# Optimization experiments

Hardware: AMD Instinct MI355X
Metric: run time of the kernel (lower is better)

## Reference

```python
import jax, jax.numpy as jnp
import numpy as np

N = 100000      # num nodes
E = 1600000     # num edges
F_IN = 128
F_OUT = 128
BN_EPS = 1e-5


def setup_inputs() -> dict:
    key = jax.random.key(0)
    ks = jax.random.split(key, 8)
    x = jax.random.normal(ks[0], (N, F_IN), dtype=jnp.float32)
    edge_index = jax.random.randint(ks[1], (2, E), 0, N, dtype=jnp.int64)
    # GIN learnable epsilon (init 0.0)
    eps = jnp.zeros((), dtype=jnp.float32)
    # MLP: Linear(F_IN->F_OUT) -> BatchNorm1d -> ReLU -> Linear(F_OUT->F_OUT)
    lim1 = 1.0 / np.sqrt(F_IN)
    W1 = jax.random.uniform(ks[2], (F_OUT, F_IN), minval=-lim1, maxval=lim1, dtype=jnp.float32)
    b1 = jax.random.uniform(ks[3], (F_OUT,), minval=-lim1, maxval=lim1, dtype=jnp.float32)
    gamma = jnp.ones((F_OUT,), dtype=jnp.float32)
    beta = jnp.zeros((F_OUT,), dtype=jnp.float32)
    lim2 = 1.0 / np.sqrt(F_OUT)
    W2 = jax.random.uniform(ks[4], (F_OUT, F_OUT), minval=-lim2, maxval=lim2, dtype=jnp.float32)
    b2 = jax.random.uniform(ks[5], (F_OUT,), minval=-lim2, maxval=lim2, dtype=jnp.float32)
    return {"x": x, "edge_index": edge_index, "eps": eps,
            "W1": W1, "b1": b1, "gamma": gamma, "beta": beta,
            "W2": W2, "b2": b2}


def reference(x, edge_index, eps, W1, b1, gamma, beta, W2, b2):
    row, col = edge_index[0], edge_index[1]
    # gather neighbor features and scatter-add into destination nodes
    agg = jax.ops.segment_sum(x[col], row, num_segments=x.shape[0])  # [N, F_IN]
    h = (1.0 + eps) * x + agg
    # Linear 1
    h = h @ W1.T + b1  # [N, F_OUT]
    # BatchNorm1d (training mode: batch stats over nodes, biased variance)
    mu = jnp.mean(h, axis=0)
    var = jnp.mean(jnp.square(h - mu), axis=0)
    h = (h - mu) * jax.lax.rsqrt(var + BN_EPS) * gamma + beta
    h = jax.nn.relu(h)
    # Linear 2
    return h @ W2.T + b2
```

## Files before the change

### kernel.cpp

```cpp
#include <hip/hip_runtime.h>


#define F 128
#define NPB 64

typedef __attribute__((ext_vector_type(8))) short short8;
typedef __attribute__((ext_vector_type(4))) float float4v;

__device__ inline float b2f(unsigned short u) {
    union { unsigned int i; float f; } v; v.i = ((unsigned int)u) << 16; return v.f;
}
__device__ inline unsigned short f2b(float f) {
    union { float f; unsigned int i; } v; v.f = f;
    unsigned int r = v.i + 0x7FFFu + ((v.i >> 16) & 1u);
    return (unsigned short)(r >> 16);
}

__global__ __launch_bounds__(256) void conv_kernel(const float* __restrict__ x,
                                                   unsigned short* __restrict__ xh, int total,
                                                   const float* __restrict__ W1,
                                                   const float* __restrict__ W2,
                                                   unsigned short* __restrict__ w1h,
                                                   unsigned short* __restrict__ w2h,
                                                   int* __restrict__ bucketCnt, int nbuk,
                                                   float* __restrict__ stats) {
    int t = blockIdx.x * 256 + threadIdx.x;
    int i = t * 8;
    if (i < total) {
        float4 v0 = *(const float4*)(x + i);
        float4 v1 = *(const float4*)(x + i + 4);
        short8 o;
        o[0] = (short)f2b(v0.x); o[1] = (short)f2b(v0.y); o[2] = (short)f2b(v0.z); o[3] = (short)f2b(v0.w);
        o[4] = (short)f2b(v1.x); o[5] = (short)f2b(v1.y); o[6] = (short)f2b(v1.z); o[7] = (short)f2b(v1.w);
        *(short8*)(xh + i) = o;
    }
    if (t < F * F) {
        w1h[t] = f2b(W1[t]);
        w2h[t] = f2b(W2[t]);
    }
    if (blockIdx.x == 0) {
        for (int k = threadIdx.x; k < nbuk; k += 256) bucketCnt[k] = 0;
    } else if (blockIdx.x == 1) {
        if (threadIdx.x < 256) stats[threadIdx.x] = 0.f;
    }
}

__global__ __launch_bounds__(256) void bucket_hist_kernel(const int* __restrict__ rows,
                                                          int* __restrict__ bucketCnt,
                                                          int E, int nbuk) {
    extern __shared__ int bh[];
    int tid = threadIdx.x;
    for (int i = tid; i < nbuk; i += 256) bh[i] = 0;
    __syncthreads();
    int stride = gridDim.x * 256;
    for (int i = blockIdx.x * 256 + tid; i < E; i += stride)
        atomicAdd(&bh[rows[i] >> 6], 1);
    __syncthreads();
    for (int b = tid; b < nbuk; b += 256) {
        int c = bh[b];
        if (c) atomicAdd(&bucketCnt[b], c);
    }
}

__global__ void scan_buckets_kernel(const int* __restrict__ bucketCnt, int* __restrict__ bOffs,
                                    int* __restrict__ gcursor, int nbuk) {
    const int SEG = 7;
    __shared__ int tmp[256];
    int t = threadIdx.x;
    int base = t * SEG;
    int v[SEG], s = 0;
#pragma unroll
    for (int j = 0; j < SEG; j++) {
        int idx = base + j;
        v[j] = (idx < nbuk) ? bucketCnt[idx] : 0;
        s += v[j];
    }
    tmp[t] = s;
    __syncthreads();
    for (int off = 1; off < 256; off <<= 1) {
        int u = (t >= off) ? tmp[t - off] : 0;
        __syncthreads();
        tmp[t] += u;
        __syncthreads();
    }
    int run = tmp[t] - s;
#pragma unroll
    for (int j = 0; j < SEG; j++) {
        int idx = base + j;
        if (idx < nbuk) { bOffs[idx] = run; gcursor[idx] = run; }
        run += v[j];
    }
    if (t == 255) bOffs[nbuk] = tmp[255];
}

__global__ __launch_bounds__(1024) void binned_scatter_kernel(const int* __restrict__ rows,
                                                              const int* __restrict__ cols,
                                                              int* __restrict__ gcursor,
                                                              int* __restrict__ recbuf,
                                                              int E, int nbuk) {
    extern __shared__ int sm[];
    int* bh = sm;
    int* gb = sm + nbuk;
    int tid = threadIdx.x;
    int chunk = (E + gridDim.x - 1) / gridDim.x;
    int e0 = blockIdx.x * chunk;
    int e1 = min(E, e0 + chunk);
    for (int i = tid; i < nbuk; i += 1024) bh[i] = 0;
    __syncthreads();
    for (int i = e0 + tid; i < e1; i += 1024)
        atomicAdd(&bh[rows[i] >> 6], 1);
    __syncthreads();
    for (int b = tid; b < nbuk; b += 1024) {
        int c = bh[b];
        gb[b] = c ? atomicAdd(&gcursor[b], c) : 0;
        bh[b] = 0;
    }
    __syncthreads();
    for (int i = e0 + tid; i < e1; i += 1024) {
        int r = rows[i], c = cols[i];
        int k = r >> 6;
        int rk = atomicAdd(&bh[k], 1);
        recbuf[gb[k] + rk] = (c << 6) | (r & 63);
    }
}

__global__ __launch_bounds__(256) void bucket_sort_kernel(const int* __restrict__ recbuf,
                                                          const int* __restrict__ bOffs,
                                                          int* __restrict__ clist,
                                                          int* __restrict__ offs,
                                                          int n, int nbuk) {
    __shared__ int hist[NPB];
    __shared__ int cur[NPB];
    int b = blockIdx.x, tid = threadIdx.x;
    int base = bOffs[b];
    int cnt = bOffs[b + 1] - base;
    if (tid < NPB) hist[tid] = 0;
    __syncthreads();
    for (int i = tid; i < cnt; i += 256) atomicAdd(&hist[recbuf[base + i] & 63], 1);
    __syncthreads();
    if (tid < 64) {
        int h = hist[tid], v = h;
#pragma unroll
        for (int off = 1; off < 64; off <<= 1) {
            int u = __shfl_up(v, off, 64);
            if (tid >= off) v += u;
        }
        cur[tid] = v - h;
        int g = b * NPB + tid;
        if (g < n) offs[g] = base + v - h;
    }
    if (b == 0 && tid == 0) offs[n] = bOffs[nbuk];
    __syncthreads();
    for (int i = tid; i < cnt; i += 256) {
        int r = recbuf[base + i];
        int p = atomicAdd(&cur[r & 63], 1);
        clist[base + p] = r >> 6;
    }
}

__global__ __launch_bounds__(256) void agg_kernel(const unsigned short* __restrict__ xh,
                                                  const int* __restrict__ offs,
                                                  const int* __restrict__ clist,
                                                  const float* __restrict__ epsPtr,
                                                  unsigned short* __restrict__ h0h,
                                                  int base_node, int n_end) {
    int wave = threadIdx.x >> 6, lane = threadIdx.x & 63;
    int node = base_node + blockIdx.x * 4 + wave;
    if (node >= n_end) return;
    int qt = lane >> 4;
    int c16 = lane & 15;
    const short8* xh8 = (const short8*)xh;
    float acc[8];
#pragma unroll
    for (int j = 0; j < 8; j++) acc[j] = 0.f;
    int s = offs[node], e = offs[node + 1];
    int i = s;
    for (; i + 16 <= e; i += 16) {
        int c[4];
#pragma unroll
        for (int u = 0; u < 4; u++) c[u] = clist[i + 4 * u + qt];
        short8 v[4];
#pragma unroll
        for (int u = 0; u < 4; u++) v[u] = xh8[(size_t)c[u] * 16 + c16];
#pragma unroll
        for (int u = 0; u < 4; u++)
#pragma unroll
            for (int j = 0; j < 8; j++) acc[j] += b2f((unsigned short)v[u][j]);
    }
    if (i < e) {
        int c[4];
#pragma unroll
        for (int u = 0; u < 4; u++) {
            int idx = i + 4 * u + qt;
            c[u] = (idx < e) ? clist[idx] : -1;
        }
        short8 v[4];
#pragma unroll
        for (int u = 0; u < 4; u++)
            v[u] = xh8[(size_t)(c[u] < 0 ? 0 : c[u]) * 16 + c16];
#pragma unroll
        for (int u = 0; u < 4; u++) {
            if (c[u] >= 0) {
#pragma unroll
                for (int j = 0; j < 8; j++) acc[j] += b2f((unsigned short)v[u][j]);
            }
        }
    }
#pragma unroll
    for (int j = 0; j < 8; j++) {
        acc[j] += __shfl_xor(acc[j], 16, 64);
        acc[j] += __shfl_xor(acc[j], 32, 64);
    }
    if (qt == 0) {
        float sc = 1.0f + epsPtr[0];
        short8 xv = xh8[(size_t)node * 16 + c16];
        short8 o;
#pragma unroll
        for (int j = 0; j < 8; j++) {
            float r = fmaf(sc, b2f((unsigned short)xv[j]), acc[j]);
            o[j] = (short)f2b(r);
        }
        ((short8*)h0h)[(size_t)node * 16 + c16] = o;
    }
}

#define WLD 136
__global__ __launch_bounds__(256, 2) void gemm1_mfma_kernel(const unsigned short* __restrict__ h0h,
                                                            const unsigned short* __restrict__ w1h,
                                                            const float* __restrict__ b1,
                                                            unsigned short* __restrict__ h1h,
                                                            float* __restrict__ partials, int n) {
    __shared__ unsigned short wl[128 * WLD];
    __shared__ float red[4 * 256];
    int tid = threadIdx.x;
    for (int i = tid; i < 128 * 16; i += 256) {
        int r = i >> 4, ch = i & 15;
        *(short8*)(wl + r * WLD + ch * 8) = *(const short8*)(w1h + r * 128 + ch * 8);
    }
    __syncthreads();

    int wv = tid >> 6, lane = tid & 63;
    int q = lane >> 4, c15 = lane & 15;
    int rowbase = blockIdx.x * 64 + wv * 16;
    int arow = rowbase + c15; if (arow >= n) arow = n - 1;
    const unsigned short* aptr = h0h + (size_t)arow * 128 + q * 8;

    float4v acc[8];
#pragma unroll
    for (int nt = 0; nt < 8; nt++) {
        float bb = b1[nt * 16 + c15];
        acc[nt] = (float4v){bb, bb, bb, bb};
    }
#pragma unroll
    for (int ks = 0; ks < 4; ks++) {
        short8 a = *(const short8*)(aptr + ks * 32);
        const unsigned short* wp = wl + q * 8 + ks * 32;
#pragma unroll
        for (int nt = 0; nt < 8; nt++) {
            short8 b = *(const short8*)(wp + (nt * 16 + c15) * WLD);
            acc[nt] = __builtin_amdgcn_mfma_f32_16x16x32_bf16(a, b, acc[nt], 0, 0, 0);
        }
    }

    float sum[8], sq[8];
#pragma unroll
    for (int nt = 0; nt < 8; nt++) {
        sum[nt] = 0.f; sq[nt] = 0.f;
#pragma unroll
        for (int r = 0; r < 4; r++) {
            int row = rowbase + q * 4 + r;
            if (row < n) {
                float v = acc[nt][r];
                h1h[(size_t)row * 128 + nt * 16 + c15] = f2b(v);
                sum[nt] += v; sq[nt] += v * v;
            }
        }
        sum[nt] += __shfl_xor(sum[nt], 16, 64);
        sum[nt] += __shfl_xor(sum[nt], 32, 64);
        sq[nt]  += __shfl_xor(sq[nt], 16, 64);
        sq[nt]  += __shfl_xor(sq[nt], 32, 64);
    }
    if (lane < 16) {
#pragma unroll
        for (int nt = 0; nt < 8; nt++) {
            red[wv * 256 + nt * 16 + c15] = sum[nt];
            red[wv * 256 + 128 + nt * 16 + c15] = sq[nt];
        }
    }
    __syncthreads();
    if (wv == 0) {
        float* pout = partials + (size_t)blockIdx.x * 256;
        for (int c = lane; c < 128; c += 64) {
            float S = red[c] + red[256 + c] + red[512 + c] + red[768 + c];
            float Q = red[128 + c] + red[384 + c] + red[640 + c] + red[896 + c];
            pout[c] = S;
            pout[128 + c] = Q;
        }
    }
}

__global__ __launch_bounds__(256) void bn_reduce_kernel(const float* __restrict__ partials,
                                                        float* __restrict__ stats, int nb) {
    int t = threadIdx.x;
    int per = (nb + gridDim.x - 1) / gridDim.x;
    int j0 = blockIdx.x * per, j1 = min(nb, j0 + per);
    float s = 0.f;
    for (int j = j0; j < j1; j++) s += partials[(size_t)j * 256 + t];
    atomicAdd(&stats[t], s);
}

__global__ __launch_bounds__(256, 2) void gemm2_mfma_kernel(const unsigned short* __restrict__ h1h,
                                                            const unsigned short* __restrict__ w2h,
                                                            const float* __restrict__ b2,
                                                            const float* __restrict__ stats,
                                                            const float* __restrict__ gamma,
                                                            const float* __restrict__ beta,
                                                            float* __restrict__ out, int n) {
    __shared__ unsigned short wl[128 * WLD];
    __shared__ float ssl[256];
    int tid = threadIdx.x;
    for (int i = tid; i < 128 * 16; i += 256) {
        int r = i >> 4, ch = i & 15;
        *(short8*)(wl + r * WLD + ch * 8) = *(const short8*)(w2h + r * 128 + ch * 8);
    }
    if (tid < 128) {
        float inv_n = 1.0f / (float)n;
        float mu = stats[tid] * inv_n;
        float var = stats[F + tid] * inv_n - mu * mu;
        var = fmaxf(var, 0.0f);
        float rs = rsqrtf(var + 1e-5f);
        float s = gamma[tid] * rs;
        ssl[tid] = s;
        ssl[F + tid] = beta[tid] - mu * s;
    }
    __syncthreads();

    int wv = tid >> 6, lane = tid & 63;
    int q = lane >> 4, c15 = lane & 15;
    int rowbase = blockIdx.x * 64 + wv * 16;
    int arow = rowbase + c15; if (arow >= n) arow = n - 1;
    const unsigned short* aptr = h1h + (size_t)arow * 128 + q * 8;

    float4v acc[8];
#pragma unroll
    for (int nt = 0; nt < 8; nt++) {
        float bb = b2[nt * 16 + c15];
        acc[nt] = (float4v){bb, bb, bb, bb};
    }
#pragma unroll
    for (int ks = 0; ks < 4; ks++) {
        short8 araw = *(const short8*)(aptr + ks * 32);
        const float* ssp = ssl + ks * 32 + q * 8;
        float4 s0 = *(const float4*)(ssp);
        float4 s1 = *(const float4*)(ssp + 4);
        float4 t0 = *(const float4*)(ssp + 128);
        float4 t1 = *(const float4*)(ssp + 132);
        short8 a;
        a[0] = (short)f2b(fmaxf(fmaf(b2f((unsigned short)araw[0]), s0.x, t0.x), 0.f));
        a[1] = (short)f2b(fmaxf(fmaf(b2f((unsigned short)araw[1]), s0.y, t0.y), 0.f));
        a[2] = (short)f2b(fmaxf(fmaf(b2f((unsigned short)araw[2]), s0.z, t0.z), 0.f));
        a[3] = (short)f2b(fmaxf(fmaf(b2f((unsigned short)araw[3]), s0.w, t0.w), 0.f));
        a[4] = (short)f2b(fmaxf(fmaf(b2f((unsigned short)araw[4]), s1.x, t1.x), 0.f));
        a[5] = (short)f2b(fmaxf(fmaf(b2f((unsigned short)araw[5]), s1.y, t1.y), 0.f));
        a[6] = (short)f2b(fmaxf(fmaf(b2f((unsigned short)araw[6]), s1.z, t1.z), 0.f));
        a[7] = (short)f2b(fmaxf(fmaf(b2f((unsigned short)araw[7]), s1.w, t1.w), 0.f));
        const unsigned short* wp = wl + q * 8 + ks * 32;
#pragma unroll
        for (int nt = 0; nt < 8; nt++) {
            short8 b = *(const short8*)(wp + (nt * 16 + c15) * WLD);
            acc[nt] = __builtin_amdgcn_mfma_f32_16x16x32_bf16(a, b, acc[nt], 0, 0, 0);
        }
    }
#pragma unroll
    for (int nt = 0; nt < 8; nt++) {
#pragma unroll
        for (int r = 0; r < 4; r++) {
            int row = rowbase + q * 4 + r;
            if (row < n)
                out[(size_t)row * 128 + nt * 16 + c15] = acc[nt][r];
        }
    }
}

extern "C" void kernel_launch(void* const* d_in, const int* in_sizes, int n_in,
                              void* d_out, int out_size, void* d_ws, size_t ws_size,
                              hipStream_t stream) {
    const float* x     = (const float*)d_in[0];
    const int*   ei    = (const int*)d_in[1];
    const float* eps   = (const float*)d_in[2];
    const float* W1    = (const float*)d_in[3];
    const float* b1    = (const float*)d_in[4];
    const float* gamma = (const float*)d_in[5];
    const float* beta  = (const float*)d_in[6];
    const float* W2    = (const float*)d_in[7];
    const float* b2    = (const float*)d_in[8];
    float* out = (float*)d_out;

    const int E = in_sizes[1] / 2;
    const int n = in_sizes[0] / F;
    const int nbuk = (n + NPB - 1) / NPB;
    const int ntiles = (n + 63) / 64;

    char* w = (char*)d_ws;
    auto alloc = [&](size_t bytes) -> void* {
        void* p = (void*)w;
        w += (bytes + 255) & ~(size_t)255;
        return p;
    };
    int*            bucketCnt = (int*)alloc((size_t)nbuk * 4);
    int*            bOffs     = (int*)alloc((size_t)(nbuk + 1) * 4);
    int*            gcursor   = (int*)alloc((size_t)nbuk * 4);
    int*            offs      = (int*)alloc((size_t)(n + 1) * 4);
    float*          stats     = (float*)alloc(256 * 4);
    float*          partials  = (float*)alloc((size_t)ntiles * 256 * 4);
    unsigned short* w1h       = (unsigned short*)alloc(F * F * 2);
    unsigned short* w2h       = (unsigned short*)alloc(F * F * 2);
    int*            recbuf    = (int*)alloc((size_t)E * 4);
    int*            clist     = (int*)alloc((size_t)E * 4);
    unsigned short* xh        = (unsigned short*)alloc((size_t)n * F * 2);
    unsigned short* h0h       = (unsigned short*)alloc((size_t)n * F * 2);
    unsigned short* h1h       = (unsigned short*)alloc((size_t)n * F * 2);

    const int* rows = ei;
    const int* cols = ei + E;

    conv_kernel<<<(n * F / 8 + 255) / 256, 256, 0, stream>>>(x, xh, n * F, W1, W2, w1h, w2h,
                                                             bucketCnt, nbuk, stats);
    bucket_hist_kernel<<<256, 256, nbuk * 4, stream>>>(rows, bucketCnt, E, nbuk);
    scan_buckets_kernel<<<1, 256, 0, stream>>>(bucketCnt, bOffs, gcursor, nbuk);
    binned_scatter_kernel<<<128, 1024, nbuk * 8, stream>>>(rows, cols, gcursor, recbuf, E, nbuk);
    bucket_sort_kernel<<<nbuk, 256, 0, stream>>>(recbuf, bOffs, clist, offs, n, nbuk);

    int nhalf = n / 2;
    agg_kernel<<<(nhalf + 3) / 4, 256, 0, stream>>>(xh, offs, clist, eps, h0h, 0, nhalf);
    agg_kernel<<<(n - nhalf + 3) / 4, 256, 0, stream>>>(xh, offs, clist, eps, h0h, nhalf, n);

    gemm1_mfma_kernel<<<ntiles, 256, 0, stream>>>(h0h, w1h, b1, h1h, partials, n);
    bn_reduce_kernel<<<16, 256, 0, stream>>>(partials, stats, ntiles);
    gemm2_mfma_kernel<<<ntiles, 256, 0, stream>>>(h1h, w2h, b2, stats, gamma, beta, out, n);
}
```

Measured before the change: 294.6 us.

## Replace two-level bucket sort CSR build with direct global-atomic counting sort

Replaces the bucketed histogram, binned scatter and per-bucket local sort with a per-node global atomic histogram, a chunked two-level prefix scan, and a direct scatter that uses per-node global atomics to place column indices. This drops the intermediate record buffer and one pass over the edges. In exchange it relies on 1.6M global atomics per pass, spread over 100K addresses, instead of shared-memory atomics. The split of the aggregation into two launches is also merged into one. Edge order within a row becomes nondeterministic, which can change floating-point summation order.

```diff
diff --git a/kernel.cpp b/kernel.cpp
--- a/kernel.cpp
+++ b/kernel.cpp
@@ -2,7 +2,7 @@
 
 
 #define F 128
-#define NPB 64
+#define CHK 1024
 
 typedef __attribute__((ext_vector_type(8))) short short8;
 typedef __attribute__((ext_vector_type(4))) float float4v;
@@ -22,8 +22,8 @@
                                                    const float* __restrict__ W2,
                                                    unsigned short* __restrict__ w1h,
                                                    unsigned short* __restrict__ w2h,
-                                                   int* __restrict__ bucketCnt, int nbuk,
-                                                   float* __restrict__ stats) {
+                                                   int* __restrict__ cnt, int* __restrict__ used,
+                                                   int n, float* __restrict__ stats) {
     int t = blockIdx.x * 256 + threadIdx.x;
     int i = t * 8;
     if (i < total) {
@@ -38,142 +38,97 @@
         w1h[t] = f2b(W1[t]);
         w2h[t] = f2b(W2[t]);
     }
-    if (blockIdx.x == 0) {
-        for (int k = threadIdx.x; k < nbuk; k += 256) bucketCnt[k] = 0;
-    } else if (blockIdx.x == 1) {
-        if (threadIdx.x < 256) stats[threadIdx.x] = 0.f;
-    }
-}
-
-__global__ __launch_bounds__(256) void bucket_hist_kernel(const int* __restrict__ rows,
-                                                          int* __restrict__ bucketCnt,
-                                                          int E, int nbuk) {
-    extern __shared__ int bh[];
-    int tid = threadIdx.x;
-    for (int i = tid; i < nbuk; i += 256) bh[i] = 0;
-    __syncthreads();
+    if (t < n) { cnt[t] = 0; used[t] = 0; }
+    if (t < 256 && blockIdx.x == 0) {  }
+    if (blockIdx.x == 1 && threadIdx.x < 256) stats[threadIdx.x] = 0.f;
+}
+
+__global__ __launch_bounds__(256) void edge_hist_kernel(const int* __restrict__ rows,
+                                                        int* __restrict__ cnt, int E) {
     int stride = gridDim.x * 256;
-    for (int i = blockIdx.x * 256 + tid; i < E; i += stride)
-        atomicAdd(&bh[rows[i] >> 6], 1);
-    __syncthreads();
-    for (int b = tid; b < nbuk; b += 256) {
-        int c = bh[b];
-        if (c) atomicAdd(&bucketCnt[b], c);
-    }
-}
-
-__global__ void scan_buckets_kernel(const int* __restrict__ bucketCnt, int* __restrict__ bOffs,
-                                    int* __restrict__ gcursor, int nbuk) {
-    const int SEG = 7;
-    __shared__ int tmp[256];
+    for (int i = blockIdx.x * 256 + threadIdx.x; i < E; i += stride)
+        atomicAdd(&cnt[rows[i]], 1);
+}
+
+__global__ __launch_bounds__(1024) void scan_chunk_kernel(const int* __restrict__ cnt,
+                                                          int* __restrict__ eoff,
+                                                          int* __restrict__ btot, int n) {
+    __shared__ int wsum[16];
     int t = threadIdx.x;
-    int base = t * SEG;
-    int v[SEG], s = 0;
-#pragma unroll
-    for (int j = 0; j < SEG; j++) {
-        int idx = base + j;
-        v[j] = (idx < nbuk) ? bucketCnt[idx] : 0;
-        s += v[j];
-    }
-    tmp[t] = s;
-    __syncthreads();
-    for (int off = 1; off < 256; off <<= 1) {
+    int i = blockIdx.x * CHK + t;
+    int v = (i < n) ? cnt[i] : 0;
+    int lane = t & 63, wv = t >> 6;
+    int x = v;
+#pragma unroll
+    for (int off = 1; off < 64; off <<= 1) {
+        int u = __shfl_up(x, off, 64);
+        if (lane >= off) x += u;
+    }
+    if (lane == 63) wsum[wv] = x;
+    __syncthreads();
+    if (wv == 0 && lane < 16) {
+        int w = wsum[lane];
+        int y = w;
+#pragma unroll
+        for (int off = 1; off < 16; off <<= 1) {
+            int u = __shfl_up(y, off, 64);
+            if (lane >= off) y += u;
+        }
+        wsum[lane] = y - w;
+    }
+    __syncthreads();
+    int excl = (x - v) + wsum[wv];
+    if (i <= n) eoff[i] = excl;
+    if (t == CHK - 1) btot[blockIdx.x] = excl + v;
+}
+
+__global__ void scan_base_kernel(const int* __restrict__ btot, int* __restrict__ cbase,
+                                 int nchunk) {
+    __shared__ int tmp[128];
+    int t = threadIdx.x;
+    int v = (t < nchunk) ? btot[t] : 0;
+    tmp[t] = v;
+    __syncthreads();
+    for (int off = 1; off < 128; off <<= 1) {
         int u = (t >= off) ? tmp[t - off] : 0;
         __syncthreads();
         tmp[t] += u;
         __syncthreads();
     }
-    int run = tmp[t] - s;
-#pragma unroll
-    for (int j = 0; j < SEG; j++) {
-        int idx = base + j;
-        if (idx < nbuk) { bOffs[idx] = run; gcursor[idx] = run; }
-        run += v[j];
-    }
-    if (t == 255) bOffs[nbuk] = tmp[255];
-}
-
-__global__ __launch_bounds__(1024) void binned_scatter_kernel(const int* __restrict__ rows,
-                                                              const int* __restrict__ cols,
-                                                              int* __restrict__ gcursor,
-                                                              int* __restrict__ recbuf,
-                                                              int E, int nbuk) {
-    extern __shared__ int sm[];
-    int* bh = sm;
-    int* gb = sm + nbuk;
-    int tid = threadIdx.x;
-    int chunk = (E + gridDim.x - 1) / gridDim.x;
-    int e0 = blockIdx.x * chunk;
-    int e1 = min(E, e0 + chunk);
-    for (int i = tid; i < nbuk; i += 1024) bh[i] = 0;
-    __syncthreads();
-    for (int i = e0 + tid; i < e1; i += 1024)
-        atomicAdd(&bh[rows[i] >> 6], 1);
-    __syncthreads();
-    for (int b = tid; b < nbuk; b += 1024) {
-        int c = bh[b];
-        gb[b] = c ? atomicAdd(&gcursor[b], c) : 0;
-        bh[b] = 0;
-    }
-    __syncthreads();
-    for (int i = e0 + tid; i < e1; i += 1024) {
+    if (t < nchunk) cbase[t] = tmp[t] - v;
+}
+
+__global__ __launch_bounds__(256) void scatter_kernel(const int* __restrict__ rows,
+                                                      const int* __restrict__ cols,
+                                                      const int* __restrict__ eoff,
+                                                      const int* __restrict__ cbase,
+                                                      int* __restrict__ used,
+                                                      int* __restrict__ clist, int E) {
+    int stride = gridDim.x * 256;
+    for (int i = blockIdx.x * 256 + threadIdx.x; i < E; i += stride) {
         int r = rows[i], c = cols[i];
-        int k = r >> 6;
-        int rk = atomicAdd(&bh[k], 1);
-        recbuf[gb[k] + rk] = (c << 6) | (r & 63);
-    }
-}
-
-__global__ __launch_bounds__(256) void bucket_sort_kernel(const int* __restrict__ recbuf,
-                                                          const int* __restrict__ bOffs,
-                                                          int* __restrict__ clist,
-                                                          int* __restrict__ offs,
-                                                          int n, int nbuk) {
-    __shared__ int hist[NPB];
-    __shared__ int cur[NPB];
-    int b = blockIdx.x, tid = threadIdx.x;
-    int base = bOffs[b];
-    int cnt = bOffs[b + 1] - base;
-    if (tid < NPB) hist[tid] = 0;
-    __syncthreads();
-    for (int i = tid; i < cnt; i += 256) atomicAdd(&hist[recbuf[base + i] & 63], 1);
-    __syncthreads();
-    if (tid < 64) {
-        int h = hist[tid], v = h;
-#pragma unroll
-        for (int off = 1; off < 64; off <<= 1) {
-            int u = __shfl_up(v, off, 64);
-            if (tid >= off) v += u;
-        }
-        cur[tid] = v - h;
-        int g = b * NPB + tid;
-        if (g < n) offs[g] = base + v - h;
-    }
-    if (b == 0 && tid == 0) offs[n] = bOffs[nbuk];
-    __syncthreads();
-    for (int i = tid; i < cnt; i += 256) {
-        int r = recbuf[base + i];
-        int p = atomicAdd(&cur[r & 63], 1);
-        clist[base + p] = r >> 6;
+        int rank = atomicAdd(&used[r], 1);
+        clist[eoff[r] + cbase[r >> 10] + rank] = c;
     }
 }
 
 __global__ __launch_bounds__(256) void agg_kernel(const unsigned short* __restrict__ xh,
-                                                  const int* __restrict__ offs,
+                                                  const int* __restrict__ eoff,
+                                                  const int* __restrict__ cbase,
                                                   const int* __restrict__ clist,
                                                   const float* __restrict__ epsPtr,
-                                                  unsigned short* __restrict__ h0h,
-                                                  int base_node, int n_end) {
+                                                  unsigned short* __restrict__ h0h, int n) {
     int wave = threadIdx.x >> 6, lane = threadIdx.x & 63;
-    int node = base_node + blockIdx.x * 4 + wave;
-    if (node >= n_end) return;
+    int node = blockIdx.x * 4 + wave;
+    if (node >= n) return;
     int qt = lane >> 4;
     int c16 = lane & 15;
     const short8* xh8 = (const short8*)xh;
     float acc[8];
 #pragma unroll
     for (int j = 0; j < 8; j++) acc[j] = 0.f;
-    int s = offs[node], e = offs[node + 1];
+    int s = eoff[node] + cbase[node >> 10];
+    int e = eoff[node + 1] + cbase[(node + 1) >> 10];
     int i = s;
     for (; i + 16 <= e; i += 16) {
         int c[4];
@@ -398,7 +353,7 @@
 
     const int E = in_sizes[1] / 2;
     const int n = in_sizes[0] / F;
-    const int nbuk = (n + NPB - 1) / NPB;
+    const int nchunk = n / CHK + 1;
     const int ntiles = (n + 63) / 64;
 
     char* w = (char*)d_ws;
@@ -407,33 +362,30 @@
         w += (bytes + 255) & ~(size_t)255;
         return p;
     };
-    int*            bucketCnt = (int*)alloc((size_t)nbuk * 4);
-    int*            bOffs     = (int*)alloc((size_t)(nbuk + 1) * 4);
-    int*            gcursor   = (int*)alloc((size_t)nbuk * 4);
-    int*            offs      = (int*)alloc((size_t)(n + 1) * 4);
-    float*          stats     = (float*)alloc(256 * 4);
-    float*          partials  = (float*)alloc((size_t)ntiles * 256 * 4);
-    unsigned short* w1h       = (unsigned short*)alloc(F * F * 2);
-    unsigned short* w2h       = (unsigned short*)alloc(F * F * 2);
-    int*            recbuf    = (int*)alloc((size_t)E * 4);
-    int*            clist     = (int*)alloc((size_t)E * 4);
-    unsigned short* xh        = (unsigned short*)alloc((size_t)n * F * 2);
-    unsigned short* h0h       = (unsigned short*)alloc((size_t)n * F * 2);
-    unsigned short* h1h       = (unsigned short*)alloc((size_t)n * F * 2);
+    int*            cnt      = (int*)alloc((size_t)n * 4);
+    int*            used     = (int*)alloc((size_t)n * 4);
+    int*            eoff     = (int*)alloc((size_t)(n + 2) * 4);
+    int*            btot     = (int*)alloc((size_t)nchunk * 4);
+    int*            cbase    = (int*)alloc((size_t)nchunk * 4);
+    float*          stats    = (float*)alloc(256 * 4);
+    float*          partials = (float*)alloc((size_t)ntiles * 256 * 4);
+    unsigned short* w1h      = (unsigned short*)alloc(F * F * 2);
+    unsigned short* w2h      = (unsigned short*)alloc(F * F * 2);
+    int*            clist    = (int*)alloc((size_t)E * 4);
+    unsigned short* xh       = (unsigned short*)alloc((size_t)n * F * 2);
+    unsigned short* h0h      = (unsigned short*)alloc((size_t)n * F * 2);
+    unsigned short* h1h      = (unsigned short*)alloc((size_t)n * F * 2);
 
     const int* rows = ei;
     const int* cols = ei + E;
 
     conv_kernel<<<(n * F / 8 + 255) / 256, 256, 0, stream>>>(x, xh, n * F, W1, W2, w1h, w2h,
-                                                             bucketCnt, nbuk, stats);
-    bucket_hist_kernel<<<256, 256, nbuk * 4, stream>>>(rows, bucketCnt, E, nbuk);
-    scan_buckets_kernel<<<1, 256, 0, stream>>>(bucketCnt, bOffs, gcursor, nbuk);
-    binned_scatter_kernel<<<128, 1024, nbuk * 8, stream>>>(rows, cols, gcursor, recbuf, E, nbuk);
-    bucket_sort_kernel<<<nbuk, 256, 0, stream>>>(recbuf, bOffs, clist, offs, n, nbuk);
-
-    int nhalf = n / 2;
-    agg_kernel<<<(nhalf + 3) / 4, 256, 0, stream>>>(xh, offs, clist, eps, h0h, 0, nhalf);
-    agg_kernel<<<(n - nhalf + 3) / 4, 256, 0, stream>>>(xh, offs, clist, eps, h0h, nhalf, n);
+                                                             cnt, used, n, stats);
+    edge_hist_kernel<<<1024, 256, 0, stream>>>(rows, cnt, E);
+    scan_chunk_kernel<<<nchunk, CHK, 0, stream>>>(cnt, eoff, btot, n);
+    scan_base_kernel<<<1, 128, 0, stream>>>(btot, cbase, nchunk);
+    scatter_kernel<<<1024, 256, 0, stream>>>(rows, cols, eoff, cbase, used, clist, E);
+    agg_kernel<<<(n + 3) / 4, 256, 0, stream>>>(xh, eoff, cbase, clist, eps, h0h, n);
 
     gemm1_mfma_kernel<<<ntiles, 256, 0, stream>>>(h0h, w1h, b1, h1h, partials, n);
     bn_reduce_kernel<<<16, 256, 0, stream>>>(partials, stats, ntiles);
```

After: 384.4 us. +30.5%, slower.

## Stage binned scatter records in LDS and write contiguous per-bucket runs

Applied to the files above, without the earlier changes.

The binned scatter kernel now does a block-local prefix scan over bucket counts and places each edge record into a shared-memory staging buffer sorted by bucket. It then reserves global space per bucket and copies each bucket's run to recbuf with coalesced wavefront writes, replacing the previous scattered global stores. The grid grows so each block's edges fit the LDS capacity. The cost is large static shared memory (about 63KB), which lowers occupancy, plus extra scan and sync work, and it relies on nbuk staying within the fixed NBUKMAX bound.

```diff
diff --git a/kernel.cpp b/kernel.cpp
--- a/kernel.cpp
+++ b/kernel.cpp
@@ -3,6 +3,8 @@
 
 #define F 128
 #define NPB 64
+#define NBUKMAX 1600
+#define RECCAP 12544
 
 typedef __attribute__((ext_vector_type(8))) short short8;
 typedef __attribute__((ext_vector_type(4))) float float4v;
@@ -98,29 +100,70 @@
                                                               int* __restrict__ gcursor,
                                                               int* __restrict__ recbuf,
                                                               int E, int nbuk) {
-    extern __shared__ int sm[];
-    int* bh = sm;
-    int* gb = sm + nbuk;
+    __shared__ int cur[NBUKMAX];
+    __shared__ int lb[NBUKMAX + 1];
+    __shared__ int recs[RECCAP];
+    __shared__ int wsum[17];
     int tid = threadIdx.x;
+    int lane = tid & 63, wv = tid >> 6;
     int chunk = (E + gridDim.x - 1) / gridDim.x;
     int e0 = blockIdx.x * chunk;
     int e1 = min(E, e0 + chunk);
-    for (int i = tid; i < nbuk; i += 1024) bh[i] = 0;
+    for (int k = tid; k < nbuk; k += 1024) cur[k] = 0;
     __syncthreads();
     for (int i = e0 + tid; i < e1; i += 1024)
-        atomicAdd(&bh[rows[i] >> 6], 1);
-    __syncthreads();
-    for (int b = tid; b < nbuk; b += 1024) {
-        int c = bh[b];
-        gb[b] = c ? atomicAdd(&gcursor[b], c) : 0;
-        bh[b] = 0;
-    }
+        atomicAdd(&cur[rows[i] >> 6], 1);
+    __syncthreads();
+    {
+        int i0 = 2 * tid, i1 = 2 * tid + 1;
+        int c0 = (i0 < nbuk) ? cur[i0] : 0;
+        int c1 = (i1 < nbuk) ? cur[i1] : 0;
+        int s = c0 + c1;
+        int x = s;
+#pragma unroll
+        for (int off = 1; off < 64; off <<= 1) {
+            int u = __shfl_up(x, off, 64);
+            if (lane >= off) x += u;
+        }
+        if (lane == 63) wsum[wv] = x;
+        __syncthreads();
+        if (wv == 0 && lane < 16) {
+            int w0 = wsum[lane];
+            int y = w0;
+#pragma unroll
+            for (int off = 1; off < 16; off <<= 1) {
+                int u = __shfl_up(y, off, 64);
+                if (lane >= off) y += u;
+            }
+            wsum[lane] = y - w0;
+        }
+        __syncthreads();
+        int bse = wsum[wv] + (x - s);
+        if (i0 <= nbuk) lb[i0] = bse;
+        if (i1 <= nbuk) lb[i1] = bse + c0;
+        if (i1 + 1 == nbuk || (i1 == nbuk - 1)) lb[nbuk] = bse + c0 + c1;
+        if (i0 == nbuk - 1) lb[nbuk] = bse + c0;
+    }
+    __syncthreads();
+    for (int k = tid; k < nbuk; k += 1024) cur[k] = lb[k];
     __syncthreads();
     for (int i = e0 + tid; i < e1; i += 1024) {
         int r = rows[i], c = cols[i];
         int k = r >> 6;
-        int rk = atomicAdd(&bh[k], 1);
-        recbuf[gb[k] + rk] = (c << 6) | (r & 63);
+        int p = atomicAdd(&cur[k], 1);
+        recs[p] = (c << 6) | (r & 63);
+    }
+    __syncthreads();
+    for (int k = tid; k < nbuk; k += 1024) {
+        int c = lb[k + 1] - lb[k];
+        cur[k] = c ? atomicAdd(&gcursor[k], c) : 0;
+    }
+    __syncthreads();
+    for (int k = wv; k < nbuk; k += 16) {
+        int s = lb[k], e = lb[k + 1];
+        int g = cur[k];
+        for (int j = s + lane; j < e; j += 64)
+            recbuf[g + (j - s)] = recs[j];
     }
 }
 
@@ -400,6 +443,8 @@
     const int n = in_sizes[0] / F;
     const int nbuk = (n + NPB - 1) / NPB;
     const int ntiles = (n + 63) / 64;
+    int SB = (E + RECCAP - 1) / RECCAP;
+    if (SB < 128) SB = 128;
 
     char* w = (char*)d_ws;
     auto alloc = [&](size_t bytes) -> void* {
@@ -428,7 +473,7 @@
                                                              bucketCnt, nbuk, stats);
     bucket_hist_kernel<<<256, 256, nbuk * 4, stream>>>(rows, bucketCnt, E, nbuk);
     scan_buckets_kernel<<<1, 256, 0, stream>>>(bucketCnt, bOffs, gcursor, nbuk);
-    binned_scatter_kernel<<<128, 1024, nbuk * 8, stream>>>(rows, cols, gcursor, recbuf, E, nbuk);
+    binned_scatter_kernel<<<SB, 1024, 0, stream>>>(rows, cols, gcursor, recbuf, E, nbuk);
     bucket_sort_kernel<<<nbuk, 256, 0, stream>>>(recbuf, bOffs, clist, offs, n, nbuk);
 
     int nhalf = n / 2;
```

New measurement: 293.4 us. Within noise of the previous version (-0.4%).
